# Performance work log

Measured on AMD Instinct MI355X. Metric: run time of the kernel, lower is better.

## Reference

```python
import jax, jax.numpy as jnp
import numpy as np

PRIOR = 0.2
TEMP = 1.0
THRESHOLD = 0.5
B, L, D, H = 8, 4096, 768, 512


def setup_inputs() -> dict:
    key = jax.random.key(0)
    k1, k2, k3, k4 = jax.random.split(key, 4)
    hidden = jax.random.normal(k1, (B, L, D), jnp.float32)
    # MLP params: Linear(D,H) -> ReLU -> Linear(H,1)
    W1 = jax.random.normal(k2, (D, H), jnp.float32) / np.sqrt(D).astype(np.float32)
    b1 = jnp.zeros((H,), jnp.float32)
    W2 = jax.random.normal(k3, (H, 1), jnp.float32) / np.sqrt(H).astype(np.float32)
    b2 = jnp.zeros((1,), jnp.float32)
    # pre-sampled uniform noise for the RelaxedBernoulli logistic reparameterization
    noise_u = jax.random.uniform(k4, (B, L), jnp.float32, minval=1e-6, maxval=1.0 - 1e-6)
    return dict(hidden=hidden, W1=W1, b1=b1, W2=W2, b2=b2, noise_u=noise_u)


def reference(hidden, W1, b1, W2, b2, noise_u):
    bs, seq_len, model_dim = hidden.shape
    # boundary MLP -> per-token logits [B, L]
    h = jax.nn.relu(jnp.einsum('bld,dh->blh', hidden, W1) + b1)
    logits = (jnp.einsum('blh,ho->blo', h, W2) + b2)[..., 0]
    # RelaxedBernoulli rsample: sigmoid((logits + logistic_noise) / temp),
    # since logit(sigmoid(logits)) == logits
    logistic_noise = jnp.log(noise_u) - jnp.log1p(-noise_u)
    soft_boundaries = jax.nn.sigmoid((logits + logistic_noise) / TEMP)
    hard_bin = (soft_boundaries > THRESHOLD).astype(soft_boundaries.dtype)
    # straight-through estimator
    hard_boundaries = soft_boundaries + jax.lax.stop_gradient(hard_bin - soft_boundaries)
    # segment id of each token: number of boundaries strictly before it
    # (boundary token is the last element of its segment)
    seg = (jnp.cumsum(hard_bin, axis=1) - hard_bin).astype(jnp.int32)  # [B, L] in [0, L)
    ids = (seg + seq_len * jnp.arange(bs, dtype=jnp.int32)[:, None]).reshape(-1)
    flat = hidden.reshape(bs * seq_len, model_dim)
    seg_sum = jax.ops.segment_sum(flat, ids, num_segments=bs * seq_len)
    seg_cnt = jax.ops.segment_sum(jnp.ones((bs * seq_len,), hidden.dtype), ids,
                                  num_segments=bs * seq_len)
    # mean pooling per segment; unused segment slots stay zero (padded to L segments,
    # equivalent to the torch [S,B,D]->transpose output up to zero padding)
    pooled = (seg_sum / jnp.maximum(seg_cnt, 1.0)[:, None]).reshape(bs, seq_len, model_dim)
    # hinge loss on boundary rate: penalize |rate - (prior+0.05)| beyond margin 0.05
    ratio = jnp.mean(hard_boundaries)
    loss = jax.nn.relu(jnp.abs(ratio - (PRIOR + 0.05)) - 0.05)
    num_boundaries = jnp.sum(hard_bin)
    total_positions = jnp.asarray(bs * seq_len, jnp.float32)
    return pooled, loss, num_boundaries, total_positions
```

## Files before the change

### kernel.cpp

```cpp
#include <hip/hip_runtime.h>
#include <math.h>

typedef __attribute__((ext_vector_type(8))) short short8;
typedef __attribute__((ext_vector_type(4))) float float4v;
typedef unsigned int uint;

#define BATCH 8
#define SEQ   4096
#define DIM   768
#define HID   512
#define M_TOK (BATCH * SEQ)

static __device__ __forceinline__ short f2bf_rne(float x) {
    unsigned int u = __float_as_uint(x);
    unsigned int r = (u + 0x7FFFu + ((u >> 16) & 1u)) >> 16;
    return (short)r;
}
static __device__ __forceinline__ uint pack_bf2(float a, float b) {
    return __builtin_amdgcn_perm(__float_as_uint(b), __float_as_uint(a), 0x07060302u);
}
union FragU { uint u[4]; short8 s; };
static __device__ __forceinline__ void gl2lds16(const void* g, void* l) {
    __builtin_amdgcn_global_load_lds(
        (const __attribute__((address_space(1))) unsigned int*)g,
        (__attribute__((address_space(3))) unsigned int*)l, 16, 0, 0);
}

__global__ __launch_bounds__(256) void prep_kernel(const float* __restrict__ W1,
                                                   short* __restrict__ W1T) {
    __shared__ float t[64][65];
    const int bk = blockIdx.x % 12, bn = blockIdx.x / 12;
    const int k0 = bk * 64, n0 = bn * 64;
    const int tr = threadIdx.x >> 6, tc = threadIdx.x & 63;
#pragma unroll
    for (int i = 0; i < 16; i++) {
        int k = tr + i * 4;
        t[k][tc] = W1[(size_t)(k0 + k) * HID + n0 + tc];
    }
    __syncthreads();
#pragma unroll
    for (int i = 0; i < 16; i++) {
        int n = tr + i * 4;
        W1T[(size_t)(n0 + n) * DIM + k0 + tc] = f2bf_rne(t[tc][n]);
    }
}

#define MLP_BM    128
#define MLP_STEPS 24
#define MLP_ABYTES 16384
#define MLP_BBYTES 32768
#define MLP_BUF   (MLP_ABYTES + MLP_BBYTES)
#define MLP_LDS   (2 * MLP_BUF)

__global__ __launch_bounds__(512, 2) void mlp_kernel(const float* __restrict__ A,
                                                     const short* __restrict__ BT,
                                                     const float* __restrict__ b1,
                                                     const float* __restrict__ W2,
                                                     float* __restrict__ logits) {
    extern __shared__ char smem[];
    const int tid = threadIdx.x, wave = tid >> 6, lane = tid & 63;
    const int q = lane >> 4, r = lane & 15;
    const int wr = wave >> 2, wc = wave & 3;
    const int m0 = blockIdx.x * MLP_BM;

    const float* aS0 = A + (size_t)(m0 + wave * 16 + r) * DIM + q * 8;
    const float* aS1 = aS0 + 4;
    const int aD0 = wave * 2048, aD1 = wave * 2048 + 1024;
    const short* bS[4];
    int bD[4];
#pragma unroll
    for (int j = 0; j < 4; j++) {
        int h = wave * 4 + j;
        bS[j] = BT + (size_t)(h * 16 + r) * DIM + q * 8;
        bD[j] = MLP_ABYTES + h * 1024;
    }

    float4v acc[4][8] = {};

    gl2lds16(aS0, smem + aD0);
    gl2lds16(aS1, smem + aD1);
#pragma unroll
    for (int j = 0; j < 4; j++) gl2lds16(bS[j], smem + bD[j]);
    __syncthreads();

    for (int p = 0; p < MLP_STEPS; ++p) {
        if (p + 1 < MLP_STEPS) {
            char* nb = smem + ((p + 1) & 1) * MLP_BUF;
            const int ko = (p + 1) * 32;
            gl2lds16(aS0 + ko, nb + aD0);
            gl2lds16(aS1 + ko, nb + aD1);
#pragma unroll
            for (int j = 0; j < 4; j++) gl2lds16(bS[j] + ko, nb + bD[j]);
        }
        char* base = smem + (p & 1) * MLP_BUF;

        short8 bfr[8];
#pragma unroll
        for (int nf = 0; nf < 8; nf++)
            bfr[nf] = *(const short8*)(base + MLP_ABYTES + (wc * 8 + nf) * 1024 + lane * 16);
#pragma unroll
        for (int mf = 0; mf < 4; mf++) {
            const int g = wr * 4 + mf;
            float4v f0 = *(const float4v*)(base + g * 2048 + lane * 16);
            float4v f1 = *(const float4v*)(base + g * 2048 + 1024 + lane * 16);
            FragU af;
            af.u[0] = pack_bf2(f0[0], f0[1]);
            af.u[1] = pack_bf2(f0[2], f0[3]);
            af.u[2] = pack_bf2(f1[0], f1[1]);
            af.u[3] = pack_bf2(f1[2], f1[3]);
#pragma unroll
            for (int nf = 0; nf < 8; nf++)
                acc[mf][nf] = __builtin_amdgcn_mfma_f32_16x16x32_bf16(
                    af.s, bfr[nf], acc[mf][nf], 0, 0, 0);
        }
        __syncthreads();
    }

    float b1v[8], w2v[8];
#pragma unroll
    for (int nf = 0; nf < 8; nf++) {
        int gc = wc * 128 + nf * 16 + r;
        b1v[nf] = b1[gc];
        w2v[nf] = W2[gc];
    }
    float* red = (float*)smem;
#pragma unroll
    for (int mf = 0; mf < 4; mf++)
#pragma unroll
        for (int v = 0; v < 4; v++) {
            float pp = 0.f;
#pragma unroll
            for (int nf = 0; nf < 8; nf++) {
                float hh = acc[mf][nf][v] + b1v[nf];
                hh = hh > 0.f ? hh : 0.f;
                pp += hh * w2v[nf];
            }
#pragma unroll
            for (int off = 1; off < 16; off <<= 1) pp += __shfl_xor(pp, off, 64);
            if (r == 0) red[wc * 128 + wr * 64 + mf * 16 + q * 4 + v] = pp;
        }
    __syncthreads();
    if (tid < 128) {
        logits[m0 + tid] = red[tid] + red[128 + tid] + red[256 + tid] + red[384 + tid];
    }
}

__global__ __launch_bounds__(1024) void boundary_kernel(const float* __restrict__ logits,
                                                        const float* __restrict__ b2p,
                                                        const float* __restrict__ noise,
                                                        int* __restrict__ starts,
                                                        int* __restrict__ nseg,
                                                        int* __restrict__ nbcount) {
    const int b = blockIdx.x, tid = threadIdx.x;
    const int base = tid * 4;
    const float b2 = b2p[0];
    int h[4], c = 0;
#pragma unroll
    for (int j = 0; j < 4; j++) {
        int l = base + j;
        float u = noise[b * SEQ + l];
        float lg = logits[b * SEQ + l] + b2 + logf(u) - log1pf(-u);
        h[j] = (lg > 0.f) ? 1 : 0;
        c += h[j];
    }
    const int lane = tid & 63, wid = tid >> 6;
    int inc = c;
    for (int off = 1; off < 64; off <<= 1) {
        int t = __shfl_up(inc, off, 64);
        if (lane >= off) inc += t;
    }
    __shared__ int wtot[16], woff[16], extra[2];
    if (lane == 63) wtot[wid] = inc;
    if (tid == 1023) extra[0] = h[3];
    __syncthreads();
    if (tid == 0) {
        int s = 0;
        for (int i = 0; i < 16; i++) { woff[i] = s; s += wtot[i]; }
        extra[1] = s;
    }
    __syncthreads();
    int run = (inc - c) + woff[wid];
#pragma unroll
    for (int j = 0; j < 4; j++) {
        int l = base + j;
        if (h[j]) {
            run++;
            if (l < SEQ - 1) starts[b * (SEQ + 1) + run] = l + 1;
        }
    }
    if (tid == 0) {
        int total = extra[1];
        int ns = total + (extra[0] ? 0 : 1);
        starts[b * (SEQ + 1)] = 0;
        starts[b * (SEQ + 1) + ns] = SEQ;
        nseg[b] = ns;
        nbcount[b] = total;
    }
}

__global__ __launch_bounds__(256) void pool_kernel(const float* __restrict__ hidden,
                                                   const int* __restrict__ starts,
                                                   const int* __restrict__ nseg,
                                                   float* __restrict__ out) {
    const int wid = threadIdx.x >> 6, lane = threadIdx.x & 63;
    const int s = blockIdx.x * 4 + wid, b = blockIdx.y;
    float* orow = out + (size_t)(b * SEQ + s) * DIM;
    float4v a0 = {0.f, 0.f, 0.f, 0.f}, a1 = a0, a2 = a0;
    const int ns = nseg[b];
    if (s < ns) {
        const int st = starts[b * (SEQ + 1) + s];
        const int en = starts[b * (SEQ + 1) + s + 1];
        float4v c0 = a0, c1 = a0, c2 = a0;
        const float* hbase = hidden + (size_t)(b * SEQ) * DIM;
        int row = st;
        for (; row + 2 <= en; row += 2) {
            const float* h0 = hbase + (size_t)row * DIM;
            const float* h1 = h0 + DIM;
            a0 += *(const float4v*)(h0 + lane * 4);
            a1 += *(const float4v*)(h0 + (lane + 64) * 4);
            a2 += *(const float4v*)(h0 + (lane + 128) * 4);
            c0 += *(const float4v*)(h1 + lane * 4);
            c1 += *(const float4v*)(h1 + (lane + 64) * 4);
            c2 += *(const float4v*)(h1 + (lane + 128) * 4);
        }
        if (row < en) {
            const float* h0 = hbase + (size_t)row * DIM;
            a0 += *(const float4v*)(h0 + lane * 4);
            a1 += *(const float4v*)(h0 + (lane + 64) * 4);
            a2 += *(const float4v*)(h0 + (lane + 128) * 4);
        }
        a0 += c0; a1 += c1; a2 += c2;
        const float invc = 1.f / (float)(en - st);
        a0 *= invc; a1 *= invc; a2 *= invc;
    }
    __builtin_nontemporal_store(a0, (float4v*)(orow + lane * 4));
    __builtin_nontemporal_store(a1, (float4v*)(orow + (lane + 64) * 4));
    __builtin_nontemporal_store(a2, (float4v*)(orow + (lane + 128) * 4));
}

__global__ void finalize_kernel(const int* __restrict__ nbcount, float* __restrict__ tail) {
    int nb = 0;
    for (int i = 0; i < BATCH; i++) nb += nbcount[i];
    float ratio = (float)nb / (float)M_TOK;
    float d = fabsf(ratio - 0.25f) - 0.05f;
    tail[0] = d > 0.f ? d : 0.f;
    tail[1] = (float)nb;
    tail[2] = (float)M_TOK;
}

extern "C" void kernel_launch(void* const* d_in, const int* in_sizes, int n_in,
                              void* d_out, int out_size, void* d_ws, size_t ws_size,
                              hipStream_t stream) {
    const float* hidden = (const float*)d_in[0];
    const float* W1     = (const float*)d_in[1];
    const float* b1     = (const float*)d_in[2];
    const float* W2     = (const float*)d_in[3];
    const float* b2     = (const float*)d_in[4];
    const float* noise  = (const float*)d_in[5];

    char* ws = (char*)d_ws;
    short* W1T    = (short*)(ws);
    float* logits = (float*)(ws + 786432);
    int*   starts = (int*)(ws + 917504);
    int*   nseg   = (int*)(ws + 917504 + 131104);
    int*   nbcount = nseg + 8;
    float* out    = (float*)d_out;

    static bool s_mlp_attr = false;
    if (!s_mlp_attr) {
        hipFuncSetAttribute(reinterpret_cast<const void*>(mlp_kernel),
                            hipFuncAttributeMaxDynamicSharedMemorySize, MLP_LDS);
        s_mlp_attr = true;
    }

    prep_kernel<<<96, 256, 0, stream>>>(W1, W1T);
    mlp_kernel<<<M_TOK / MLP_BM, 512, MLP_LDS, stream>>>(hidden, W1T, b1, W2, logits);
    boundary_kernel<<<BATCH, 1024, 0, stream>>>(logits, b2, noise, starts, nseg, nbcount);
    pool_kernel<<<dim3(SEQ / 4, BATCH), 256, 0, stream>>>(hidden, starts, nseg, out);
    finalize_kernel<<<1, 1, 0, stream>>>(nbcount, out + (size_t)M_TOK * DIM);
}
```

Before: 246.0 us.

## Load MLP GEMM operands directly from global into registers, drop LDS staging

The MLP GEMM no longer stages A and W1 tiles through double-buffered LDS with global_load_lds and per-step barriers. Each wave now loads its A fragments and pre-swizzled bf16 B fragments straight from global memory into registers. The prep kernel is rewritten to write W1 in MFMA fragment order so that B loads are contiguous per lane. This removes LDS traffic and barrier stalls, but A rows are re-read by the four column waves and B by the two row waves. It also loses the prefetch overlap, so the kernel now depends on L2/cache hits and compiler scheduling to hide global load latency.

```diff
diff --git a/kernel.cpp b/kernel.cpp
--- a/kernel.cpp
+++ b/kernel.cpp
@@ -20,100 +20,71 @@
     return __builtin_amdgcn_perm(__float_as_uint(b), __float_as_uint(a), 0x07060302u);
 }
 union FragU { uint u[4]; short8 s; };
-static __device__ __forceinline__ void gl2lds16(const void* g, void* l) {
-    __builtin_amdgcn_global_load_lds(
-        (const __attribute__((address_space(1))) unsigned int*)g,
-        (__attribute__((address_space(3))) unsigned int*)l, 16, 0, 0);
-}
-
-__global__ __launch_bounds__(256) void prep_kernel(const float* __restrict__ W1,
-                                                   short* __restrict__ W1T) {
-    __shared__ float t[64][65];
-    const int bk = blockIdx.x % 12, bn = blockIdx.x / 12;
-    const int k0 = bk * 64, n0 = bn * 64;
-    const int tr = threadIdx.x >> 6, tc = threadIdx.x & 63;
-#pragma unroll
-    for (int i = 0; i < 16; i++) {
-        int k = tr + i * 4;
-        t[k][tc] = W1[(size_t)(k0 + k) * HID + n0 + tc];
-    }
-    __syncthreads();
-#pragma unroll
-    for (int i = 0; i < 16; i++) {
-        int n = tr + i * 4;
-        W1T[(size_t)(n0 + n) * DIM + k0 + tc] = f2bf_rne(t[tc][n]);
-    }
-}
-
-#define MLP_BM    128
-#define MLP_STEPS 24
-#define MLP_ABYTES 16384
-#define MLP_BBYTES 32768
-#define MLP_BUF   (MLP_ABYTES + MLP_BBYTES)
-#define MLP_LDS   (2 * MLP_BUF)
+
+__global__ __launch_bounds__(64) void prep_kernel(const float* __restrict__ W1,
+                                                  short* __restrict__ W1T) {
+    const int bid = blockIdx.x;
+    const int h = bid / 24, kg = bid % 24;
+    const int lane = threadIdx.x & 63, q = lane >> 4, r = lane & 15;
+    float f[8];
+#pragma unroll
+    for (int j = 0; j < 8; j++)
+        f[j] = W1[(size_t)(kg * 32 + q * 8 + j) * HID + h * 16 + r];
+    uint u[4];
+#pragma unroll
+    for (int i = 0; i < 4; i++)
+        u[i] = ((uint)(unsigned short)f2bf_rne(f[2 * i + 1]) << 16) |
+               (uint)(unsigned short)f2bf_rne(f[2 * i]);
+    uint* dst = (uint*)(W1T + (size_t)bid * 512) + lane * 4;
+    dst[0] = u[0]; dst[1] = u[1]; dst[2] = u[2]; dst[3] = u[3];
+}
 
 __global__ __launch_bounds__(512, 2) void mlp_kernel(const float* __restrict__ A,
                                                      const short* __restrict__ BT,
                                                      const float* __restrict__ b1,
                                                      const float* __restrict__ W2,
                                                      float* __restrict__ logits) {
-    extern __shared__ char smem[];
+    __shared__ float red[512];
     const int tid = threadIdx.x, wave = tid >> 6, lane = tid & 63;
     const int q = lane >> 4, r = lane & 15;
     const int wr = wave >> 2, wc = wave & 3;
-    const int m0 = blockIdx.x * MLP_BM;
-
-    const float* aS0 = A + (size_t)(m0 + wave * 16 + r) * DIM + q * 8;
-    const float* aS1 = aS0 + 4;
-    const int aD0 = wave * 2048, aD1 = wave * 2048 + 1024;
-    const short* bS[4];
-    int bD[4];
-#pragma unroll
-    for (int j = 0; j < 4; j++) {
-        int h = wave * 4 + j;
-        bS[j] = BT + (size_t)(h * 16 + r) * DIM + q * 8;
-        bD[j] = MLP_ABYTES + h * 1024;
-    }
+    const int m0 = blockIdx.x * 128;
+
+    const float* aRow[4];
+#pragma unroll
+    for (int mf = 0; mf < 4; mf++)
+        aRow[mf] = A + (size_t)(m0 + wr * 64 + mf * 16 + r) * DIM + q * 8;
+    const short* bBase[8];
+#pragma unroll
+    for (int nf = 0; nf < 8; nf++)
+        bBase[nf] = BT + ((size_t)(wc * 8 + nf) * 24) * 512 + lane * 8;
 
     float4v acc[4][8] = {};
 
-    gl2lds16(aS0, smem + aD0);
-    gl2lds16(aS1, smem + aD1);
-#pragma unroll
-    for (int j = 0; j < 4; j++) gl2lds16(bS[j], smem + bD[j]);
-    __syncthreads();
-
-    for (int p = 0; p < MLP_STEPS; ++p) {
-        if (p + 1 < MLP_STEPS) {
-            char* nb = smem + ((p + 1) & 1) * MLP_BUF;
-            const int ko = (p + 1) * 32;
-            gl2lds16(aS0 + ko, nb + aD0);
-            gl2lds16(aS1 + ko, nb + aD1);
-#pragma unroll
-            for (int j = 0; j < 4; j++) gl2lds16(bS[j] + ko, nb + bD[j]);
-        }
-        char* base = smem + (p & 1) * MLP_BUF;
-
-        short8 bfr[8];
-#pragma unroll
-        for (int nf = 0; nf < 8; nf++)
-            bfr[nf] = *(const short8*)(base + MLP_ABYTES + (wc * 8 + nf) * 1024 + lane * 16);
-#pragma unroll
-        for (int mf = 0; mf < 4; mf++) {
-            const int g = wr * 4 + mf;
-            float4v f0 = *(const float4v*)(base + g * 2048 + lane * 16);
-            float4v f1 = *(const float4v*)(base + g * 2048 + 1024 + lane * 16);
-            FragU af;
-            af.u[0] = pack_bf2(f0[0], f0[1]);
-            af.u[1] = pack_bf2(f0[2], f0[3]);
-            af.u[2] = pack_bf2(f1[0], f1[1]);
-            af.u[3] = pack_bf2(f1[2], f1[3]);
+    for (int t = 0; t < 12; ++t) {
+#pragma unroll
+        for (int kk = 0; kk < 2; ++kk) {
+            const int kg = t * 2 + kk;
+            short8 bfr[8];
 #pragma unroll
             for (int nf = 0; nf < 8; nf++)
-                acc[mf][nf] = __builtin_amdgcn_mfma_f32_16x16x32_bf16(
-                    af.s, bfr[nf], acc[mf][nf], 0, 0, 0);
-        }
-        __syncthreads();
+                bfr[nf] = *(const short8*)(bBase[nf] + kg * 512);
+#pragma unroll
+            for (int mf = 0; mf < 4; mf++) {
+                const float* ap = aRow[mf] + kg * 32;
+                float4v f0 = *(const float4v*)(ap);
+                float4v f1 = *(const float4v*)(ap + 4);
+                FragU af;
+                af.u[0] = pack_bf2(f0[0], f0[1]);
+                af.u[1] = pack_bf2(f0[2], f0[3]);
+                af.u[2] = pack_bf2(f1[0], f1[1]);
+                af.u[3] = pack_bf2(f1[2], f1[3]);
+#pragma unroll
+                for (int nf = 0; nf < 8; nf++)
+                    acc[mf][nf] = __builtin_amdgcn_mfma_f32_16x16x32_bf16(
+                        af.s, bfr[nf], acc[mf][nf], 0, 0, 0);
+            }
+        }
     }
 
     float b1v[8], w2v[8];
@@ -123,7 +94,6 @@
         b1v[nf] = b1[gc];
         w2v[nf] = W2[gc];
     }
-    float* red = (float*)smem;
 #pragma unroll
     for (int mf = 0; mf < 4; mf++)
 #pragma unroll
@@ -266,15 +236,8 @@
     int*   nbcount = nseg + 8;
     float* out    = (float*)d_out;
 
-    static bool s_mlp_attr = false;
-    if (!s_mlp_attr) {
-        hipFuncSetAttribute(reinterpret_cast<const void*>(mlp_kernel),
-                            hipFuncAttributeMaxDynamicSharedMemorySize, MLP_LDS);
-        s_mlp_attr = true;
-    }
-
-    prep_kernel<<<96, 256, 0, stream>>>(W1, W1T);
-    mlp_kernel<<<M_TOK / MLP_BM, 512, MLP_LDS, stream>>>(hidden, W1T, b1, W2, logits);
+    prep_kernel<<<768, 64, 0, stream>>>(W1, W1T);
+    mlp_kernel<<<M_TOK / 128, 512, 0, stream>>>(hidden, W1T, b1, W2, logits);
     boundary_kernel<<<BATCH, 1024, 0, stream>>>(logits, b2, noise, starts, nseg, nbcount);
     pool_kernel<<<dim3(SEQ / 4, BATCH), 256, 0, stream>>>(hidden, starts, nseg, out);
     finalize_kernel<<<1, 1, 0, stream>>>(nbcount, out + (size_t)M_TOK * DIM);
```

Measured after the change: 269.3 us. +9.4%, slower.
